# Kernel tuning notes

Measured on AMD Instinct MI355X. Metric: run time of the kernel, lower is better.

## Reference

```python
import jax, jax.numpy as jnp
import numpy as np

B, N, NE = 64, 512, 500
FIELD_DIM, E_DIM, HIDDEN, LATENT = 256, 64, 512, 256


def _lin_init(key, fan_in, fan_out):
    kw, kb = jax.random.split(key)
    s = 1.0 / np.sqrt(fan_in)
    W = jax.random.uniform(kw, (fan_in, fan_out), minval=-s, maxval=s, dtype=jnp.float32)
    b = jax.random.uniform(kb, (fan_out,), minval=-s, maxval=s, dtype=jnp.float32)
    return W, b


def setup_inputs() -> dict:
    key = jax.random.key(0)
    ks = jax.random.split(key, 16)
    inp = {}
    inp['field_atom_lat'] = jax.random.normal(ks[0], (B, N, FIELD_DIM), dtype=jnp.float32)
    inp['mask'] = jax.random.randint(ks[1], (B, N), 0, 2).astype(bool)
    inp['e_feat'] = jax.random.normal(ks[2], (NE, E_DIM), dtype=jnp.float32)
    # query MLP (3 layers): e_dim -> hidden -> hidden -> latent
    inp['q_w1'], inp['q_b1'] = _lin_init(ks[3], E_DIM, HIDDEN)
    inp['q_w2'], inp['q_b2'] = _lin_init(ks[4], HIDDEN, HIDDEN)
    inp['q_w3'], inp['q_b3'] = _lin_init(ks[5], HIDDEN, LATENT)
    # key MLP (3 layers): field_dim -> hidden -> hidden -> latent
    inp['k_w1'], inp['k_b1'] = _lin_init(ks[6], FIELD_DIM, HIDDEN)
    inp['k_w2'], inp['k_b2'] = _lin_init(ks[7], HIDDEN, HIDDEN)
    inp['k_w3'], inp['k_b3'] = _lin_init(ks[8], HIDDEN, LATENT)
    # value MLP (3 layers)
    inp['v_w1'], inp['v_b1'] = _lin_init(ks[9], FIELD_DIM, HIDDEN)
    inp['v_w2'], inp['v_b2'] = _lin_init(ks[10], HIDDEN, HIDDEN)
    inp['v_w3'], inp['v_b3'] = _lin_init(ks[11], HIDDEN, LATENT)
    # out MLP (2 layers): latent -> hidden -> latent
    inp['o_w1'], inp['o_b1'] = _lin_init(ks[12], LATENT, HIDDEN)
    inp['o_w2'], inp['o_b2'] = _lin_init(ks[13], HIDDEN, LATENT)
    return inp


def _mlp3(x, w1, b1, w2, b2, w3, b3):
    h = jax.nn.silu(x @ w1 + b1)
    h = jax.nn.silu(h @ w2 + b2)
    return h @ w3 + b3


def _mlp2(x, w1, b1, w2, b2):
    return jax.nn.silu(x @ w1 + b1) @ w2 + b2


def reference(field_atom_lat, mask, e_feat,
              q_w1, q_b1, q_w2, q_b2, q_w3, q_b3,
              k_w1, k_b1, k_w2, k_b2, k_w3, k_b3,
              v_w1, v_b1, v_w2, v_b2, v_w3, v_b3,
              o_w1, o_b1, o_w2, o_b2):
    latent_dim = q_w3.shape[1]
    scale = latent_dim ** (-0.5)
    q = _mlp3(e_feat, q_w1, q_b1, q_w2, q_b2, q_w3, q_b3)          # [nE, L] (shared across batch)
    k = _mlp3(field_atom_lat, k_w1, k_b1, k_w2, k_b2, k_w3, k_b3)  # [B, N, L]
    v = _mlp3(field_atom_lat, v_w1, v_b1, v_w2, v_b2, v_w3, v_b3)  # [B, N, L]
    scores = jnp.einsum('el,bnl->ben', q, k) * scale               # [B, nE, N]
    scores = jnp.where(mask[:, None, :], scores, jnp.float32(-1e9))
    attn = jax.nn.softmax(scores, axis=2)
    attn = attn * mask[:, None, :].astype(attn.dtype)              # post-softmax mask, as in torch
    out = jnp.einsum('ben,bnl->bel', attn, v)                      # [B, nE, L]
    return _mlp2(out, o_w1, o_b1, o_w2, o_b2)
```

## Files before the change

kernel.cpp:

```cpp
#include <hip/hip_runtime.h>
#include <math.h>

#define BATCH 64
#define N_ATOMS 512
#define NE 500
#define FIELD_DIM 256
#define E_DIM 64
#define HIDDEN 512
#define LATENT 256

typedef short bf16x8 __attribute__((ext_vector_type(8)));
typedef unsigned short u16x8 __attribute__((ext_vector_type(8)));
typedef unsigned short u16x4 __attribute__((ext_vector_type(4)));
typedef float f32x4 __attribute__((ext_vector_type(4)));

__device__ __forceinline__ unsigned short f2bf(float x) {
    unsigned u = __float_as_uint(x);
    unsigned r = (u + 0x7FFFu + ((u >> 16) & 1u)) >> 16;
    return (unsigned short)r;
}
__device__ __forceinline__ float bf2f(unsigned short b) {
    return __uint_as_float(((unsigned)b) << 16);
}
__device__ __forceinline__ float silu_f(float x) { return x / (1.f + __expf(-x)); }

#define GLOAD_LDS16(gptr, lptr)                                                   \
    __builtin_amdgcn_global_load_lds(                                             \
        (const __attribute__((address_space(1))) void*)(gptr),                    \
        (__attribute__((address_space(3))) void*)(lptr), 16, 0, 0)

#define QW1 0
#define QW2 32768
#define QW3 294912
#define KW1 425984
#define KW2 557056
#define KW3 819200
#define VW1 950272
#define VW2 1081344
#define VW3 1343488
#define OW1 1474560
#define OW2 1605632

template <int K, bool SILU>
__device__ __forceinline__ void mlp_layer_ip(
    const unsigned short* __restrict__ Wg, const float* __restrict__ Bg,
    unsigned short* buf, int wave, int lane, int fr, int fq)
{
    constexpr int NS = K / 32;
    const int fb = wave * 64;
    const unsigned short* wp = Wg + (long long)(wave * 4) * NS * 512 + lane * 8;

    f32x4 acc[4][4];
#pragma unroll
    for (int mf = 0; mf < 4; mf++)
#pragma unroll
        for (int nf = 0; nf < 4; nf++) acc[mf][nf] = (f32x4)0.f;

    bf16x8 wfA[4];
#pragma unroll
    for (int mf = 0; mf < 4; mf++)
        wfA[mf] = *reinterpret_cast<const bf16x8*>(wp + (long long)mf * NS * 512);

#pragma unroll
    for (int ks = 0; ks < NS; ks++) {
        bf16x8 wfB[4];
        if (ks + 1 < NS) {
#pragma unroll
            for (int mf = 0; mf < 4; mf++)
                wfB[mf] = *reinterpret_cast<const bf16x8*>(
                    wp + ((long long)mf * NS + (ks + 1)) * 512);
        }
        bf16x8 bfr[4];
#pragma unroll
        for (int nf = 0; nf < 4; nf++) {
            int row = nf * 16 + fr;
            bfr[nf] = *reinterpret_cast<const bf16x8*>(
                (const char*)buf + row * (K * 2) +
                ((ks * 64 + fq * 16) ^ ((row & 7) << 4)));
        }
        __builtin_amdgcn_s_setprio(1);
#pragma unroll
        for (int mf = 0; mf < 4; mf++)
#pragma unroll
            for (int nf = 0; nf < 4; nf++)
                acc[mf][nf] = __builtin_amdgcn_mfma_f32_16x16x32_bf16(
                    wfA[mf], bfr[nf], acc[mf][nf], 0, 0, 0);
        __builtin_amdgcn_s_setprio(0);
        if (ks + 1 < NS) {
#pragma unroll
            for (int mf = 0; mf < 4; mf++) wfA[mf] = wfB[mf];
        }
    }
    __syncthreads();

#pragma unroll
    for (int mf = 0; mf < 4; mf++) {
        f32x4 bv = *reinterpret_cast<const f32x4*>(Bg + fb + mf * 16 + fq * 4);
#pragma unroll
        for (int nf = 0; nf < 4; nf++) {
            int row = nf * 16 + fr;
            u16x4 ov;
#pragma unroll
            for (int r = 0; r < 4; r++) {
                float x = acc[mf][nf][r] + bv[r];
                if (SILU) x = silu_f(x);
                ov[r] = f2bf(x);
            }
            *reinterpret_cast<u16x4*>(
                (char*)buf + row * 1024 +
                ((fb * 2 + mf * 32 + fq * 8) ^ ((row & 7) << 4))) = ov;
        }
    }
    __syncthreads();
}

template <int K, bool SILU>
__device__ __forceinline__ void mlp_layer_io(
    const unsigned short* __restrict__ Wg, const float* __restrict__ Bg,
    const unsigned short* inb, unsigned short* outb, int wave, int lane,
    int fr, int fq)
{
    constexpr int NS = K / 32;
    const int fb = wave * 64;
    const unsigned short* wp = Wg + (long long)(wave * 4) * NS * 512 + lane * 8;

    f32x4 acc[4][4];
#pragma unroll
    for (int mf = 0; mf < 4; mf++)
#pragma unroll
        for (int nf = 0; nf < 4; nf++) acc[mf][nf] = (f32x4)0.f;

    bf16x8 wfA[4];
#pragma unroll
    for (int mf = 0; mf < 4; mf++)
        wfA[mf] = *reinterpret_cast<const bf16x8*>(wp + (long long)mf * NS * 512);

#pragma unroll
    for (int ks = 0; ks < NS; ks++) {
        bf16x8 wfB[4];
        if (ks + 1 < NS) {
#pragma unroll
            for (int mf = 0; mf < 4; mf++)
                wfB[mf] = *reinterpret_cast<const bf16x8*>(
                    wp + ((long long)mf * NS + (ks + 1)) * 512);
        }
        bf16x8 bfr[4];
#pragma unroll
        for (int nf = 0; nf < 4; nf++) {
            int row = nf * 16 + fr;
            bfr[nf] = *reinterpret_cast<const bf16x8*>(
                (const char*)inb + row * (K * 2) +
                ((ks * 64 + fq * 16) ^ ((row & 7) << 4)));
        }
        __builtin_amdgcn_s_setprio(1);
#pragma unroll
        for (int mf = 0; mf < 4; mf++)
#pragma unroll
            for (int nf = 0; nf < 4; nf++)
                acc[mf][nf] = __builtin_amdgcn_mfma_f32_16x16x32_bf16(
                    wfA[mf], bfr[nf], acc[mf][nf], 0, 0, 0);
        __builtin_amdgcn_s_setprio(0);
        if (ks + 1 < NS) {
#pragma unroll
            for (int mf = 0; mf < 4; mf++) wfA[mf] = wfB[mf];
        }
    }

#pragma unroll
    for (int mf = 0; mf < 4; mf++) {
        f32x4 bv = *reinterpret_cast<const f32x4*>(Bg + fb + mf * 16 + fq * 4);
#pragma unroll
        for (int nf = 0; nf < 4; nf++) {
            int row = nf * 16 + fr;
            u16x4 ov;
#pragma unroll
            for (int r = 0; r < 4; r++) {
                float x = acc[mf][nf][r] + bv[r];
                if (SILU) x = silu_f(x);
                ov[r] = f2bf(x);
            }
            *reinterpret_cast<u16x4*>(
                (char*)outb + row * 1024 +
                ((fb * 2 + mf * 32 + fq * 8) ^ ((row & 7) << 4))) = ov;
        }
    }
    __syncthreads();
}

__device__ __forceinline__ void mlp_final512(
    const unsigned short* __restrict__ Wg, const float* __restrict__ Bg,
    const unsigned short* buf, int wave, int lane, int fr, int fq,
    f32x4 (&acc)[2][4])
{
    const int fb = wave * 32;
    const unsigned short* wp = Wg + (long long)(wave * 2) * 16 * 512 + lane * 8;
#pragma unroll
    for (int mf = 0; mf < 2; mf++)
#pragma unroll
        for (int nf = 0; nf < 4; nf++) acc[mf][nf] = (f32x4)0.f;

    bf16x8 wfA[2];
#pragma unroll
    for (int mf = 0; mf < 2; mf++)
        wfA[mf] = *reinterpret_cast<const bf16x8*>(wp + (long long)mf * 16 * 512);

#pragma unroll
    for (int ks = 0; ks < 16; ks++) {
        bf16x8 wfB[2];
        if (ks + 1 < 16) {
#pragma unroll
            for (int mf = 0; mf < 2; mf++)
                wfB[mf] = *reinterpret_cast<const bf16x8*>(
                    wp + ((long long)mf * 16 + (ks + 1)) * 512);
        }
        bf16x8 bfr[4];
#pragma unroll
        for (int nf = 0; nf < 4; nf++) {
            int row = nf * 16 + fr;
            bfr[nf] = *reinterpret_cast<const bf16x8*>(
                (const char*)buf + row * 1024 +
                ((ks * 64 + fq * 16) ^ ((row & 7) << 4)));
        }
        __builtin_amdgcn_s_setprio(1);
#pragma unroll
        for (int mf = 0; mf < 2; mf++)
#pragma unroll
            for (int nf = 0; nf < 4; nf++)
                acc[mf][nf] = __builtin_amdgcn_mfma_f32_16x16x32_bf16(
                    wfA[mf], bfr[nf], acc[mf][nf], 0, 0, 0);
        __builtin_amdgcn_s_setprio(0);
        if (ks + 1 < 16) {
#pragma unroll
            for (int mf = 0; mf < 2; mf++) wfA[mf] = wfB[mf];
        }
    }
#pragma unroll
    for (int mf = 0; mf < 2; mf++) {
        f32x4 bv = *reinterpret_cast<const f32x4*>(Bg + fb + mf * 16 + fq * 4);
#pragma unroll
        for (int nf = 0; nf < 4; nf++)
#pragma unroll
            for (int r = 0; r < 4; r++) acc[mf][nf][r] += bv[r];
    }
}

__global__ __launch_bounds__(512, 2) void fused_qkv(
    const unsigned short* __restrict__ field_bf,
    const unsigned short* __restrict__ efeat_bf,
    const unsigned short* __restrict__ wt,
    const float* __restrict__ qb1, const float* __restrict__ qb2,
    const float* __restrict__ qb3, const float* __restrict__ kb1,
    const float* __restrict__ kb2, const float* __restrict__ kb3,
    const float* __restrict__ vb1, const float* __restrict__ vb2,
    const float* __restrict__ vb3,
    unsigned short* __restrict__ qbuf,
    unsigned short* __restrict__ kbuf,
    unsigned short* __restrict__ vtb)
{
    __shared__ unsigned short buf[64 * 512];
    const int t = threadIdx.x, wave = t >> 6, lane = t & 63;
    const int fr = lane & 15, fq = lane >> 4;
    const int bid = blockIdx.x;

    if (bid < 1024) {
        const int isv = bid >> 9;
        const int m0  = (bid & 511) * 64;
        const unsigned short* W1 = wt + (isv ? VW1 : KW1);
        const unsigned short* W2 = wt + (isv ? VW2 : KW2);
        const unsigned short* W3 = wt + (isv ? VW3 : KW3);
        const float* B1 = isv ? vb1 : kb1;
        const float* B2 = isv ? vb2 : kb2;
        const float* B3 = isv ? vb3 : kb3;

#pragma unroll
        for (int c = wave; c < 32; c += 8) {
            int gi  = c * 64 + lane;
            int row = gi >> 5;
            int g   = gi & 31;
            int gs  = (g & ~7) | ((g & 7) ^ (row & 7));
            GLOAD_LDS16(field_bf + (long long)(m0 + row) * 256 + gs * 8, buf + c * 512);
        }
        __syncthreads();

        mlp_layer_ip<256, true>(W1, B1, buf, wave, lane, fr, fq);
        mlp_layer_ip<512, true>(W2, B2, buf, wave, lane, fr, fq);
        f32x4 acc[2][4];
        mlp_final512(W3, B3, buf, wave, lane, fr, fq, acc);

        if (!isv) {
#pragma unroll
            for (int mf = 0; mf < 2; mf++)
#pragma unroll
                for (int nf = 0; nf < 4; nf++) {
                    int row = m0 + nf * 16 + fr;
                    u16x4 ov;
#pragma unroll
                    for (int r = 0; r < 4; r++) ov[r] = f2bf(acc[mf][nf][r]);
                    *reinterpret_cast<u16x4*>(
                        kbuf + (long long)row * 256 + wave * 32 + mf * 16 + fq * 4) = ov;
                }
        } else {
            __syncthreads();
#pragma unroll
            for (int mf = 0; mf < 2; mf++)
#pragma unroll
                for (int nf = 0; nf < 4; nf++) {
                    int row = nf * 16 + fr;
                    u16x4 ov;
#pragma unroll
                    for (int r = 0; r < 4; r++) ov[r] = f2bf(acc[mf][nf][r]);
                    *reinterpret_cast<u16x4*>(
                        (char*)buf + row * 512 +
                        ((wave * 64 + mf * 32 + fq * 8) ^ ((row & 7) << 4))) = ov;
                }
            __syncthreads();
            int l  = t >> 1;
            int nh = (t & 1) * 32;
            int b  = m0 >> 9, nb = m0 & 511;
            long long base = ((long long)b * 256 + l) * 512 + nb + nh;
#pragma unroll
            for (int q = 0; q < 4; q++) {
                u16x8 ov;
#pragma unroll
                for (int j = 0; j < 8; j++) {
                    int n = nh + q * 8 + j;
                    ov[j] = *reinterpret_cast<const unsigned short*>(
                        (const char*)buf + n * 512 + ((l * 2) ^ ((n & 7) << 4)));
                }
                *reinterpret_cast<u16x8*>(vtb + base + q * 8) = ov;
            }
        }
    } else {
        const int m0 = (bid - 1024) * 64;
        {
            int row = t >> 3;
            int g   = lane & 7;
            int gr  = m0 + row; if (gr >= NE) gr = NE - 1;
            int gs  = g ^ (row & 7);
            GLOAD_LDS16(efeat_bf + (long long)gr * 64 + gs * 8, buf + wave * 512);
        }
        __syncthreads();

        mlp_layer_ip<64, true>(wt + QW1, qb1, buf, wave, lane, fr, fq);
        mlp_layer_ip<512, true>(wt + QW2, qb2, buf, wave, lane, fr, fq);
        f32x4 acc[2][4];
        mlp_final512(wt + QW3, qb3, buf, wave, lane, fr, fq, acc);
#pragma unroll
        for (int mf = 0; mf < 2; mf++)
#pragma unroll
            for (int nf = 0; nf < 4; nf++) {
                int row = m0 + nf * 16 + fr;
                if (row < NE) {
                    u16x4 ov;
#pragma unroll
                    for (int r = 0; r < 4; r++) ov[r] = f2bf(acc[mf][nf][r]);
                    *reinterpret_cast<u16x4*>(
                        qbuf + (long long)row * 256 + wave * 32 + mf * 16 + fq * 4) = ov;
                }
            }
    }
}

__global__ __launch_bounds__(512, 1) void attn_fused(
    const unsigned short* __restrict__ qbuf,
    const unsigned short* __restrict__ kbuf,
    const unsigned short* __restrict__ vt,
    const int* __restrict__ mask,
    const unsigned short* __restrict__ wt,
    const float* __restrict__ ob1, const float* __restrict__ ob2,
    float* __restrict__ out)
{
    __shared__ unsigned char LDS[100352];
    unsigned short* Qs = (unsigned short*)LDS;
    unsigned short* Ks = (unsigned short*)(LDS + 32768);
    unsigned short* Ps = (unsigned short*)LDS;
    unsigned short* Vs = (unsigned short*)(LDS + 65536);
    float*          red = (float*)(LDS + 98304);
    unsigned short* oin  = (unsigned short*)(LDS + 65536);
    unsigned short* obuf = (unsigned short*)LDS;

    const int id = blockIdx.x;
    const int b  = id & 63;
    const int e0 = (id >> 6) * 64;
    const int t = threadIdx.x, wave = t >> 6;
    const int lane = t & 63, fr = lane & 15, fq = lane >> 4;
    const int tr = t >> 3, tg = t & 7;

#pragma unroll
    for (int i = 0; i < 4; i++) {
        int ge = e0 + tr; if (ge >= NE) ge = NE - 1;
        int gi = tg ^ (tr & 7);
        GLOAD_LDS16(qbuf + (long long)ge * 256 + i * 64 + gi * 8,
                    Qs + i * 4096 + wave * 512);
    }
#pragma unroll
    for (int j = 0; j < 8; j++) {
        int n  = j * 64 + tr;
        int gi = tg ^ (n & 7);
        GLOAD_LDS16(kbuf + (long long)(b * 512 + n) * 256 + gi * 8,
                    Ks + j * 4096 + wave * 512);
    }
    int mk[4];
#pragma unroll
    for (int nf = 0; nf < 4; nf++) mk[nf] = mask[b * 512 + wave * 64 + nf * 16 + fr];

    f32x4 acc[4][4];
#pragma unroll
    for (int i = 0; i < 4; i++)
#pragma unroll
        for (int j = 0; j < 4; j++) acc[i][j] = (f32x4)0.f;

    __syncthreads();

    for (int ks = 0; ks < 4; ks++) {
#pragma unroll
        for (int h = 0; h < 2; h++) {
            bf16x8 af[4], bv[4];
#pragma unroll
            for (int mf = 0; mf < 4; mf++) {
                int e = mf * 16 + fr;
                int byo = ks * 8192 + e * 128 + ((h * 64 + fq * 16) ^ ((e & 7) << 4));
                af[mf] = *(const bf16x8*)((const char*)Qs + byo);
            }
#pragma unroll
            for (int nf = 0; nf < 4; nf++) {
                int n = wave * 64 + nf * 16 + fr;
                int byo = n * 128 + ((h * 64 + fq * 16) ^ ((n & 7) << 4));
                bv[nf] = *(const bf16x8*)((const char*)Ks + byo);
            }
#pragma unroll
            for (int mf = 0; mf < 4; mf++)
#pragma unroll
                for (int nf = 0; nf < 4; nf++)
                    acc[mf][nf] = __builtin_amdgcn_mfma_f32_16x16x32_bf16(
                        af[mf], bv[nf], acc[mf][nf], 0, 0, 0);
        }
        if (ks < 3) {
            __syncthreads();
#pragma unroll
            for (int j = 0; j < 8; j++) {
                int n  = j * 64 + tr;
                int gi = tg ^ (n & 7);
                GLOAD_LDS16(kbuf + (long long)(b * 512 + n) * 256 + (ks + 1) * 64 + gi * 8,
                            Ks + j * 4096 + wave * 512);
            }
            __syncthreads();
        }
    }

    const float scale = 0.0625f;
#pragma unroll
    for (int mf = 0; mf < 4; mf++)
#pragma unroll
        for (int nf = 0; nf < 4; nf++)
#pragma unroll
            for (int r = 0; r < 4; r++)
                acc[mf][nf][r] = mk[nf] ? acc[mf][nf][r] * scale : -1e9f;

    float gm[4][4];
#pragma unroll
    for (int mf = 0; mf < 4; mf++)
#pragma unroll
        for (int r = 0; r < 4; r++) {
            float m = fmaxf(fmaxf(acc[mf][0][r], acc[mf][1][r]),
                            fmaxf(acc[mf][2][r], acc[mf][3][r]));
#pragma unroll
            for (int off = 1; off < 16; off <<= 1) m = fmaxf(m, __shfl_xor(m, off, 64));
            if (fr == 0) red[(mf * 16 + fq * 4 + r) * 8 + wave] = m;
        }
    __syncthreads();
#pragma unroll
    for (int mf = 0; mf < 4; mf++)
#pragma unroll
        for (int r = 0; r < 4; r++) {
            int row = mf * 16 + fq * 4 + r;
            float4 a = *(float4*)&red[row * 8];
            float4 c = *(float4*)&red[row * 8 + 4];
            gm[mf][r] = fmaxf(fmaxf(fmaxf(a.x, a.y), fmaxf(a.z, a.w)),
                              fmaxf(fmaxf(c.x, c.y), fmaxf(c.z, c.w)));
        }
    __syncthreads();

    float inv[4][4];
#pragma unroll
    for (int mf = 0; mf < 4; mf++)
#pragma unroll
        for (int r = 0; r < 4; r++) {
            float s = 0.f;
#pragma unroll
            for (int nf = 0; nf < 4; nf++) {
                acc[mf][nf][r] = __expf(acc[mf][nf][r] - gm[mf][r]);
                s += acc[mf][nf][r];
            }
#pragma unroll
            for (int off = 1; off < 16; off <<= 1) s += __shfl_xor(s, off, 64);
            if (fr == 0) red[(mf * 16 + fq * 4 + r) * 8 + wave] = s;
        }
    __syncthreads();
#pragma unroll
    for (int mf = 0; mf < 4; mf++)
#pragma unroll
        for (int r = 0; r < 4; r++) {
            int row = mf * 16 + fq * 4 + r;
            float4 a = *(float4*)&red[row * 8];
            float4 c = *(float4*)&red[row * 8 + 4];
            inv[mf][r] = 1.f / (a.x + a.y + a.z + a.w + c.x + c.y + c.z + c.w);
        }

#pragma unroll
    for (int mf = 0; mf < 4; mf++)
#pragma unroll
        for (int nf = 0; nf < 4; nf++)
#pragma unroll
            for (int r = 0; r < 4; r++) {
                int row = mf * 16 + fq * 4 + r;
                int c   = wave * 64 + nf * 16 + fr;
                float pv = mk[nf] ? acc[mf][nf][r] * inv[mf][r] : 0.f;
                *(unsigned short*)((char*)Ps + row * 1024 + ((c * 2) ^ ((row & 7) << 4))) =
                    f2bf(pv);
            }
    __syncthreads();

    f32x4 acc2[4][2];
#pragma unroll
    for (int i = 0; i < 4; i++)
#pragma unroll
        for (int j = 0; j < 2; j++) acc2[i][j] = (f32x4)0.f;

#pragma unroll
    for (int j = 0; j < 4; j++) {
        int l  = j * 64 + tr;
        int gi = tg ^ (l & 7);
        GLOAD_LDS16(vt + (long long)(b * 256 + l) * 512 + gi * 8,
                    Vs + j * 4096 + wave * 512);
    }
    __syncthreads();

    for (int ks = 0; ks < 8; ks++) {
#pragma unroll
        for (int h = 0; h < 2; h++) {
            bf16x8 af[4], bv[2];
#pragma unroll
            for (int mf = 0; mf < 4; mf++) {
                int e = mf * 16 + fr;
                int byo = e * 1024 + ((ks * 128 + h * 64 + fq * 16) ^ ((e & 7) << 4));
                af[mf] = *(const bf16x8*)((const char*)Ps + byo);
            }
#pragma unroll
            for (int nf = 0; nf < 2; nf++) {
                int l = wave * 32 + nf * 16 + fr;
                int byo = l * 128 + ((h * 64 + fq * 16) ^ ((l & 7) << 4));
                bv[nf] = *(const bf16x8*)((const char*)Vs + byo);
            }
#pragma unroll
            for (int mf = 0; mf < 4; mf++)
#pragma unroll
                for (int nf = 0; nf < 2; nf++)
                    acc2[mf][nf] = __builtin_amdgcn_mfma_f32_16x16x32_bf16(
                        af[mf], bv[nf], acc2[mf][nf], 0, 0, 0);
        }
        if (ks < 7) {
            __syncthreads();
#pragma unroll
            for (int j = 0; j < 4; j++) {
                int l  = j * 64 + tr;
                int gi = tg ^ (l & 7);
                GLOAD_LDS16(vt + (long long)(b * 256 + l) * 512 + (ks + 1) * 64 + gi * 8,
                            Vs + j * 4096 + wave * 512);
            }
            __syncthreads();
        }
    }

    __syncthreads();
#pragma unroll
    for (int mf = 0; mf < 4; mf++)
#pragma unroll
        for (int nf = 0; nf < 2; nf++)
#pragma unroll
            for (int r = 0; r < 4; r++) {
                int row = mf * 16 + fq * 4 + r;
                int col = wave * 32 + nf * 16 + fr;
                *(unsigned short*)((char*)oin + row * 512 +
                                   ((col * 2) ^ ((row & 7) << 4))) =
                    f2bf(acc2[mf][nf][r]);
            }
    __syncthreads();

    mlp_layer_io<256, true>(wt + OW1, ob1, oin, obuf, wave, lane, fr, fq);
    f32x4 oacc[2][4];
    mlp_final512(wt + OW2, ob2, obuf, wave, lane, fr, fq, oacc);

#pragma unroll
    for (int mf = 0; mf < 2; mf++)
#pragma unroll
        for (int nf = 0; nf < 4; nf++) {
            int e = e0 + nf * 16 + fr;
            if (e < NE)
                *reinterpret_cast<f32x4*>(
                    out + ((long long)b * NE + e) * 256 + wave * 32 + mf * 16 + fq * 4) =
                    oacc[mf][nf];
        }
}

__global__ __launch_bounds__(256) void f32_to_bf16(
    const float* __restrict__ in, unsigned short* __restrict__ out, long long n8)
{
    long long i      = (long long)blockIdx.x * 256 + threadIdx.x;
    long long stride = (long long)gridDim.x * 256;
    for (; i < n8; i += stride) {
        const float4* p = reinterpret_cast<const float4*>(in + i * 8);
        float4 a = p[0], b = p[1];
        u16x8 o;
        o[0] = f2bf(a.x); o[1] = f2bf(a.y); o[2] = f2bf(a.z); o[3] = f2bf(a.w);
        o[4] = f2bf(b.x); o[5] = f2bf(b.y); o[6] = f2bf(b.z); o[7] = f2bf(b.w);
        *reinterpret_cast<u16x8*>(out + i * 8) = o;
    }
}

__global__ __launch_bounds__(256) void wt_pack(
    const float* w0, const float* w1, const float* w2, const float* w3,
    const float* w4, const float* w5, const float* w6, const float* w7,
    const float* w8, const float* w9, const float* w10, unsigned short* dst)
{
    const int Kd[11] = {64, 512, 512, 256, 512, 512, 256, 512, 512, 256, 512};
    const int Nd[11] = {512, 512, 256, 512, 512, 256, 512, 512, 256, 512, 256};
    const long long Od[11] = {QW1, QW2, QW3, KW1, KW2, KW3, VW1, VW2, VW3, OW1, OW2};
    const int z = blockIdx.z;
    const float* src = z == 0 ? w0 : z == 1 ? w1 : z == 2 ? w2 : z == 3 ? w3 :
                       z == 4 ? w4 : z == 5 ? w5 : z == 6 ? w6 : z == 7 ? w7 :
                       z == 8 ? w8 : z == 9 ? w9 : w10;
    const int K = Kd[z], N = Nd[z];
    const int k0 = blockIdx.y * 64, n0 = blockIdx.x * 64;
    if (k0 >= K || n0 >= N) return;

    __shared__ float tf[64][65];
    const int t = threadIdx.x;
    {
        const int r = t >> 2;
        const int c0 = (t & 3) * 16;
        const float* srow = src + (long long)(k0 + r) * N + n0 + c0;
#pragma unroll
        for (int q = 0; q < 4; q++) {
            float4 xv = *reinterpret_cast<const float4*>(srow + q * 4);
            tf[r][c0 + q * 4 + 0] = xv.x;
            tf[r][c0 + q * 4 + 1] = xv.y;
            tf[r][c0 + q * 4 + 2] = xv.z;
            tf[r][c0 + q * 4 + 3] = xv.w;
        }
    }
    __syncthreads();

#pragma unroll
    for (int it = 0; it < 2; it++) {
        int wi = t + it * 256;
        int nc = wi & 63;
        int k8 = wi >> 6;
        int kg = k0 + k8 * 8;
        int ks = kg >> 5;
        int fq = (kg >> 3) & 3;
        int f16 = (n0 + nc) >> 4;
        int fr  = nc & 15;
        u16x8 ov;
#pragma unroll
        for (int e = 0; e < 8; e++) ov[e] = f2bf(tf[k8 * 8 + e][nc]);
        long long off = Od[z] +
            (((long long)f16 * (K / 32) + ks) * 64 + fq * 16 + fr) * 8;
        *reinterpret_cast<u16x8*>(dst + off) = ov;
    }
}

extern "C" void kernel_launch(void* const* d_in, const int* in_sizes, int n_in,
                              void* d_out, int out_size, void* d_ws, size_t ws_size,
                              hipStream_t stream)
{
    const float* field = (const float*)d_in[0];
    const int*   mask  = (const int*)d_in[1];
    const float* efeat = (const float*)d_in[2];
    const float* q_w1 = (const float*)d_in[3];  const float* q_b1 = (const float*)d_in[4];
    const float* q_w2 = (const float*)d_in[5];  const float* q_b2 = (const float*)d_in[6];
    const float* q_w3 = (const float*)d_in[7];  const float* q_b3 = (const float*)d_in[8];
    const float* k_w1 = (const float*)d_in[9];  const float* k_b1 = (const float*)d_in[10];
    const float* k_w2 = (const float*)d_in[11]; const float* k_b2 = (const float*)d_in[12];
    const float* k_w3 = (const float*)d_in[13]; const float* k_b3 = (const float*)d_in[14];
    const float* v_w1 = (const float*)d_in[15]; const float* v_b1 = (const float*)d_in[16];
    const float* v_w2 = (const float*)d_in[17]; const float* v_b2 = (const float*)d_in[18];
    const float* v_w3 = (const float*)d_in[19]; const float* v_b3 = (const float*)d_in[20];
    const float* o_w1 = (const float*)d_in[21]; const float* o_b1 = (const float*)d_in[22];
    const float* o_w2 = (const float*)d_in[23]; const float* o_b2 = (const float*)d_in[24];

    unsigned short* ws = (unsigned short*)d_ws;
    unsigned short* field_bf = ws;
    unsigned short* efeat_bf = ws + 8388608;
    unsigned short* wt       = ws + 8420608;
    unsigned short* qbuf     = ws + 10157312;
    unsigned short* kbuf     = ws + 10285312;
    unsigned short* vtb      = ws + 18673920;

    f32_to_bf16<<<dim3(2048), dim3(256), 0, stream>>>(field, field_bf, 1048576);
    f32_to_bf16<<<dim3(16),   dim3(256), 0, stream>>>(efeat, efeat_bf, 4000);
    wt_pack<<<dim3(8, 8, 11), dim3(256), 0, stream>>>(
        q_w1, q_w2, q_w3, k_w1, k_w2, k_w3, v_w1, v_w2, v_w3, o_w1, o_w2, wt);

    fused_qkv<<<dim3(1032), dim3(512), 0, stream>>>(
        field_bf, efeat_bf, wt, q_b1, q_b2, q_b3, k_b1, k_b2, k_b3,
        v_b1, v_b2, v_b3, qbuf, kbuf, vtb);

    attn_fused<<<dim3(512), dim3(512), 0, stream>>>(
        qbuf, kbuf, vtb, mask, wt, o_b1, o_b2, (float*)d_out);
}
```

Baseline: 210.6 us.

## Fuse fp32-to-bf16 input conversion into QKV kernel and deepen weight prefetch

The separate f32_to_bf16 kernels for field and e_feat are dropped. fused_qkv now reads the fp32 inputs directly, converts them in registers and writes bf16 into LDS, which removes an extra round trip of the 32MB field tensor through global memory and two launches. All MLP layer loops also prefetch weight fragments two k-steps ahead instead of one, to hide global load latency. In exchange, the direct global-to-LDS loads become register loads plus LDS stores, and the extra buffers raise register pressure under launch_bounds(512,2).

```diff
diff --git a/kernel.cpp b/kernel.cpp
--- a/kernel.cpp
+++ b/kernel.cpp
@@ -56,19 +56,22 @@
 #pragma unroll
         for (int nf = 0; nf < 4; nf++) acc[mf][nf] = (f32x4)0.f;
 
-    bf16x8 wfA[4];
+    bf16x8 wfA[4], wfB[4];
 #pragma unroll
     for (int mf = 0; mf < 4; mf++)
         wfA[mf] = *reinterpret_cast<const bf16x8*>(wp + (long long)mf * NS * 512);
+#pragma unroll
+    for (int mf = 0; mf < 4; mf++)
+        wfB[mf] = *reinterpret_cast<const bf16x8*>(wp + ((long long)mf * NS + 1) * 512);
 
 #pragma unroll
     for (int ks = 0; ks < NS; ks++) {
-        bf16x8 wfB[4];
-        if (ks + 1 < NS) {
+        bf16x8 wfC[4];
+        if (ks + 2 < NS) {
 #pragma unroll
             for (int mf = 0; mf < 4; mf++)
-                wfB[mf] = *reinterpret_cast<const bf16x8*>(
-                    wp + ((long long)mf * NS + (ks + 1)) * 512);
+                wfC[mf] = *reinterpret_cast<const bf16x8*>(
+                    wp + ((long long)mf * NS + (ks + 2)) * 512);
         }
         bf16x8 bfr[4];
 #pragma unroll
@@ -86,9 +89,11 @@
                 acc[mf][nf] = __builtin_amdgcn_mfma_f32_16x16x32_bf16(
                     wfA[mf], bfr[nf], acc[mf][nf], 0, 0, 0);
         __builtin_amdgcn_s_setprio(0);
-        if (ks + 1 < NS) {
-#pragma unroll
-            for (int mf = 0; mf < 4; mf++) wfA[mf] = wfB[mf];
+#pragma unroll
+        for (int mf = 0; mf < 4; mf++) wfA[mf] = wfB[mf];
+        if (ks + 2 < NS) {
+#pragma unroll
+            for (int mf = 0; mf < 4; mf++) wfB[mf] = wfC[mf];
         }
     }
     __syncthreads();
@@ -130,19 +135,22 @@
 #pragma unroll
         for (int nf = 0; nf < 4; nf++) acc[mf][nf] = (f32x4)0.f;
 
-    bf16x8 wfA[4];
+    bf16x8 wfA[4], wfB[4];
 #pragma unroll
     for (int mf = 0; mf < 4; mf++)
         wfA[mf] = *reinterpret_cast<const bf16x8*>(wp + (long long)mf * NS * 512);
+#pragma unroll
+    for (int mf = 0; mf < 4; mf++)
+        wfB[mf] = *reinterpret_cast<const bf16x8*>(wp + ((long long)mf * NS + 1) * 512);
 
 #pragma unroll
     for (int ks = 0; ks < NS; ks++) {
-        bf16x8 wfB[4];
-        if (ks + 1 < NS) {
+        bf16x8 wfC[4];
+        if (ks + 2 < NS) {
 #pragma unroll
             for (int mf = 0; mf < 4; mf++)
-                wfB[mf] = *reinterpret_cast<const bf16x8*>(
-                    wp + ((long long)mf * NS + (ks + 1)) * 512);
+                wfC[mf] = *reinterpret_cast<const bf16x8*>(
+                    wp + ((long long)mf * NS + (ks + 2)) * 512);
         }
         bf16x8 bfr[4];
 #pragma unroll
@@ -160,9 +168,11 @@
                 acc[mf][nf] = __builtin_amdgcn_mfma_f32_16x16x32_bf16(
                     wfA[mf], bfr[nf], acc[mf][nf], 0, 0, 0);
         __builtin_amdgcn_s_setprio(0);
-        if (ks + 1 < NS) {
-#pragma unroll
-            for (int mf = 0; mf < 4; mf++) wfA[mf] = wfB[mf];
+#pragma unroll
+        for (int mf = 0; mf < 4; mf++) wfA[mf] = wfB[mf];
+        if (ks + 2 < NS) {
+#pragma unroll
+            for (int mf = 0; mf < 4; mf++) wfB[mf] = wfC[mf];
         }
     }
 
@@ -199,19 +209,22 @@
 #pragma unroll
         for (int nf = 0; nf < 4; nf++) acc[mf][nf] = (f32x4)0.f;
 
-    bf16x8 wfA[2];
+    bf16x8 wfA[2], wfB[2];
 #pragma unroll
     for (int mf = 0; mf < 2; mf++)
         wfA[mf] = *reinterpret_cast<const bf16x8*>(wp + (long long)mf * 16 * 512);
+#pragma unroll
+    for (int mf = 0; mf < 2; mf++)
+        wfB[mf] = *reinterpret_cast<const bf16x8*>(wp + ((long long)mf * 16 + 1) * 512);
 
 #pragma unroll
     for (int ks = 0; ks < 16; ks++) {
-        bf16x8 wfB[2];
-        if (ks + 1 < 16) {
+        bf16x8 wfC[2];
+        if (ks + 2 < 16) {
 #pragma unroll
             for (int mf = 0; mf < 2; mf++)
-                wfB[mf] = *reinterpret_cast<const bf16x8*>(
-                    wp + ((long long)mf * 16 + (ks + 1)) * 512);
+                wfC[mf] = *reinterpret_cast<const bf16x8*>(
+                    wp + ((long long)mf * 16 + (ks + 2)) * 512);
         }
         bf16x8 bfr[4];
 #pragma unroll
@@ -229,9 +242,11 @@
                 acc[mf][nf] = __builtin_amdgcn_mfma_f32_16x16x32_bf16(
                     wfA[mf], bfr[nf], acc[mf][nf], 0, 0, 0);
         __builtin_amdgcn_s_setprio(0);
-        if (ks + 1 < 16) {
-#pragma unroll
-            for (int mf = 0; mf < 2; mf++) wfA[mf] = wfB[mf];
+#pragma unroll
+        for (int mf = 0; mf < 2; mf++) wfA[mf] = wfB[mf];
+        if (ks + 2 < 16) {
+#pragma unroll
+            for (int mf = 0; mf < 2; mf++) wfB[mf] = wfC[mf];
         }
     }
 #pragma unroll
@@ -245,8 +260,8 @@
 }
 
 __global__ __launch_bounds__(512, 2) void fused_qkv(
-    const unsigned short* __restrict__ field_bf,
-    const unsigned short* __restrict__ efeat_bf,
+    const float* __restrict__ field,
+    const float* __restrict__ efeat,
     const unsigned short* __restrict__ wt,
     const float* __restrict__ qb1, const float* __restrict__ qb2,
     const float* __restrict__ qb3, const float* __restrict__ kb1,
@@ -278,7 +293,13 @@
             int row = gi >> 5;
             int g   = gi & 31;
             int gs  = (g & ~7) | ((g & 7) ^ (row & 7));
-            GLOAD_LDS16(field_bf + (long long)(m0 + row) * 256 + gs * 8, buf + c * 512);
+            const float* p = field + (long long)(m0 + row) * 256 + gs * 8;
+            f32x4 a = *reinterpret_cast<const f32x4*>(p);
+            f32x4 b = *reinterpret_cast<const f32x4*>(p + 4);
+            u16x8 o;
+#pragma unroll
+            for (int j = 0; j < 4; j++) { o[j] = f2bf(a[j]); o[j + 4] = f2bf(b[j]); }
+            *reinterpret_cast<u16x8*>(buf + c * 512 + lane * 8) = o;
         }
         __syncthreads();
 
@@ -337,7 +358,13 @@
             int g   = lane & 7;
             int gr  = m0 + row; if (gr >= NE) gr = NE - 1;
             int gs  = g ^ (row & 7);
-            GLOAD_LDS16(efeat_bf + (long long)gr * 64 + gs * 8, buf + wave * 512);
+            const float* p = efeat + (long long)gr * 64 + gs * 8;
+            f32x4 a = *reinterpret_cast<const f32x4*>(p);
+            f32x4 b = *reinterpret_cast<const f32x4*>(p + 4);
+            u16x8 o;
+#pragma unroll
+            for (int j = 0; j < 4; j++) { o[j] = f2bf(a[j]); o[j + 4] = f2bf(b[j]); }
+            *reinterpret_cast<u16x8*>(buf + wave * 512 + lane * 8) = o;
         }
         __syncthreads();
 
@@ -601,21 +628,6 @@
                     out + ((long long)b * NE + e) * 256 + wave * 32 + mf * 16 + fq * 4) =
                     oacc[mf][nf];
         }
-}
-
-__global__ __launch_bounds__(256) void f32_to_bf16(
-    const float* __restrict__ in, unsigned short* __restrict__ out, long long n8)
-{
-    long long i      = (long long)blockIdx.x * 256 + threadIdx.x;
-    long long stride = (long long)gridDim.x * 256;
-    for (; i < n8; i += stride) {
-        const float4* p = reinterpret_cast<const float4*>(in + i * 8);
-        float4 a = p[0], b = p[1];
-        u16x8 o;
-        o[0] = f2bf(a.x); o[1] = f2bf(a.y); o[2] = f2bf(a.z); o[3] = f2bf(a.w);
-        o[4] = f2bf(b.x); o[5] = f2bf(b.y); o[6] = f2bf(b.z); o[7] = f2bf(b.w);
-        *reinterpret_cast<u16x8*>(out + i * 8) = o;
-    }
 }
 
 __global__ __launch_bounds__(256) void wt_pack(
@@ -690,20 +702,16 @@
     const float* o_w2 = (const float*)d_in[23]; const float* o_b2 = (const float*)d_in[24];
 
     unsigned short* ws = (unsigned short*)d_ws;
-    unsigned short* field_bf = ws;
-    unsigned short* efeat_bf = ws + 8388608;
     unsigned short* wt       = ws + 8420608;
     unsigned short* qbuf     = ws + 10157312;
     unsigned short* kbuf     = ws + 10285312;
     unsigned short* vtb      = ws + 18673920;
 
-    f32_to_bf16<<<dim3(2048), dim3(256), 0, stream>>>(field, field_bf, 1048576);
-    f32_to_bf16<<<dim3(16),   dim3(256), 0, stream>>>(efeat, efeat_bf, 4000);
     wt_pack<<<dim3(8, 8, 11), dim3(256), 0, stream>>>(
         q_w1, q_w2, q_w3, k_w1, k_w2, k_w3, v_w1, v_w2, v_w3, o_w1, o_w2, wt);
 
     fused_qkv<<<dim3(1032), dim3(512), 0, stream>>>(
-        field_bf, efeat_bf, wt, q_b1, q_b2, q_b3, k_b1, k_b2, k_b3,
+        field, efeat, wt, q_b1, q_b2, q_b3, k_b1, k_b2, k_b3,
         v_b1, v_b2, v_b3, qbuf, kbuf, vtb);
 
     attn_fused<<<dim3(512), dim3(512), 0, stream>>>(
```

New measurement: 207.7 us. Within noise of the previous version (-1.4%).
